# Kernel tuning notes

Hardware: AMD Instinct MI355X
Metric: run time of the kernel (lower is better)

Reference implementation:

```python
import jax, jax.numpy as jnp
import numpy as np

NV = 100000   # vehicle nodes
NE = 100000   # 'edge' nodes (dst type)
E = 250000    # graph edges (connects relation)
VDIM = 16
EDIM = 16
HID = 128
HEADS = 4
DH = 128      # out_feats per head (GATv2Conv(hid, hid))
EPS = 1e-5
NEG_SLOPE = 0.2


def _layernorm(x, g, b):
    mu = x.mean(-1, keepdims=True)
    var = ((x - mu) ** 2).mean(-1, keepdims=True)
    return (x - mu) * jax.lax.rsqrt(var + EPS) * g + b


def setup_inputs() -> dict:
    key = jax.random.key(0)
    ks = jax.random.split(key, 20)
    s = 0.05
    return {
        "v_feat": jax.random.normal(ks[0], (NV, VDIM), jnp.float32),
        "e_feat": jax.random.normal(ks[1], (NE, EDIM), jnp.float32),
        "Wv": jax.random.normal(ks[2], (VDIM, HID), jnp.float32) * s,
        "bv": jnp.zeros((HID,), jnp.float32),
        "gv": jnp.ones((HID,), jnp.float32),
        "betav": jnp.zeros((HID,), jnp.float32),
        "We": jax.random.normal(ks[3], (EDIM, HID), jnp.float32) * s,
        "be": jnp.zeros((HID,), jnp.float32),
        "ge": jnp.ones((HID,), jnp.float32),
        "betae": jnp.zeros((HID,), jnp.float32),
        "Wsrc": jax.random.normal(ks[4], (HID, HEADS * DH), jnp.float32) * s,
        "bsrc": jnp.zeros((HEADS * DH,), jnp.float32),
        "Wdst": jax.random.normal(ks[5], (HID, HEADS * DH), jnp.float32) * s,
        "bdst": jnp.zeros((HEADS * DH,), jnp.float32),
        "attn": jax.random.normal(ks[6], (HEADS, DH), jnp.float32) * s,
        "Wp": jax.random.normal(ks[7], (HID, HID), jnp.float32) * s,
        "bp": jnp.zeros((HID,), jnp.float32),
        "src": jax.random.randint(ks[8], (E,), 0, NV, jnp.int32),
        "dst": jax.random.randint(ks[9], (E,), 0, NE, jnp.int32),
    }


def reference(v_feat, e_feat, Wv, bv, gv, betav, We, be, ge, betae,
              Wsrc, bsrc, Wdst, bdst, attn, Wp, bp, src, dst):
    # --- node-type encoders: Linear -> ReLU -> LayerNorm ---
    h_v = _layernorm(jax.nn.relu(v_feat @ Wv + bv), gv, betav)      # [NV, HID]
    h_e = _layernorm(jax.nn.relu(e_feat @ We + be), ge, betae)      # [NE, HID]

    # --- GATv2Conv (bipartite: vehicle -> edge), 4 heads ---
    fs = (h_v @ Wsrc + bsrc).reshape(NV, HEADS, DH)                 # src proj
    fd = (h_e @ Wdst + bdst).reshape(NE, HEADS, DH)                 # dst proj
    e = jax.nn.leaky_relu(fs[src] + fd[dst], NEG_SLOPE)             # [E, H, D]
    score = jnp.einsum("ehd,hd->eh", e, attn)                       # [E, H]
    # segment-wise (per-dst-node) softmax over incoming edges
    smax = jax.ops.segment_max(score, dst, num_segments=NE)         # [NE, H]
    ex = jnp.exp(score - smax[dst])
    denom = jax.ops.segment_sum(ex, dst, num_segments=NE)
    alpha = ex / denom[dst]                                         # [E, H]
    out = jax.ops.segment_sum(alpha[:, :, None] * fs[src], dst,
                              num_segments=NE)                      # [NE, H, D]

    # HeteroGraphConv mean-aggregate (single relation -> identity),
    # then mean over heads (edge_out.dim()==3 branch)
    edge_out = out.mean(axis=1)                                     # [NE, HID]

    # feature_proj: Linear -> ReLU -> Dropout(eval: identity)
    return jax.nn.relu(edge_out @ Wp + bp)
```

## Files before the change

kernel.cpp:

```cpp
#include <hip/hip_runtime.h>
#include <hip/hip_bf16.h>
#include <math.h>

#define NV 100000
#define NE_N 100000
#define NEDGE 250000
#define NEG 0.2f
#define LN_EPS 1e-5f

typedef __bf16 bf16_t;
typedef __bf16 bf16x8 __attribute__((ext_vector_type(8)));
typedef float f32x4 __attribute__((ext_vector_type(4)));

__device__ inline unsigned short f2bfu(float f) {
    return __builtin_bit_cast(unsigned short, (__bf16)f);
}
__device__ inline float bfu2f(unsigned short u) {
    return (float)__builtin_bit_cast(__bf16, u);
}
__device__ inline float blo(unsigned w) { return __uint_as_float(w << 16); }
__device__ inline float bhi(unsigned w) { return __uint_as_float(w & 0xffff0000u); }
__device__ inline float lrelu(float x) { return x > 0.f ? x : NEG * x; }
__device__ inline unsigned pk2(float a, float b) {
    return (unsigned)f2bfu(a) | ((unsigned)f2bfu(b) << 16);
}

__device__ __forceinline__ void gload_lds16(const bf16_t* g, unsigned short* l) {
    __builtin_amdgcn_global_load_lds(
        (const __attribute__((address_space(1))) unsigned int*)g,
        (__attribute__((address_space(3))) unsigned int*)l,
        16, 0, 0);
}

__global__ __launch_bounds__(256) void prep_kernel(
    const float* __restrict__ Wsrc, const float* __restrict__ Wdst,
    const float* __restrict__ Wp, bf16_t* __restrict__ pS,
    bf16_t* __restrict__ pD, bf16_t* __restrict__ pP)
{
    int t = blockIdx.x * 256 + threadIdx.x;
    if (t < 8192) {
        int ksq = t >> 9, col = t & 511;
#pragma unroll
        for (int j = 0; j < 8; ++j)
            pS[(size_t)t * 8 + j] = (bf16_t)Wsrc[(ksq * 8 + j) * 512 + col];
    } else if (t < 16384) {
        int g = t - 8192;
        int ksq = g >> 9, col = g & 511;
#pragma unroll
        for (int j = 0; j < 8; ++j)
            pD[(size_t)g * 8 + j] = (bf16_t)Wdst[(ksq * 8 + j) * 512 + col];
    } else if (t < 18432) {
        int g = t - 16384;
        int ksq = g >> 7, col = g & 127;
#pragma unroll
        for (int j = 0; j < 8; ++j)
            pP[(size_t)g * 8 + j] = (bf16_t)Wp[(ksq * 8 + j) * 128 + col];
    }
}

__global__ __launch_bounds__(256) void count_kernel(
    const int* __restrict__ dst, int* __restrict__ deg)
{
    int t = blockIdx.x * 256 + threadIdx.x;
    if (t < NEDGE) atomicAdd(&deg[dst[t]], 1);
}

__global__ __launch_bounds__(256) void scan1_kernel(
    const int* __restrict__ deg, int* __restrict__ offs, int* __restrict__ bsum)
{
    __shared__ int s[256];
    int i = blockIdx.x * 256 + threadIdx.x;
    int v = (i < NE_N) ? deg[i] : 0;
    s[threadIdx.x] = v;
    __syncthreads();
    for (int off = 1; off < 256; off <<= 1) {
        int t_ = (threadIdx.x >= off) ? s[threadIdx.x - off] : 0;
        __syncthreads();
        s[threadIdx.x] += t_;
        __syncthreads();
    }
    if (i < NE_N) offs[i] = s[threadIdx.x] - v;
    if (threadIdx.x == 255) bsum[blockIdx.x] = s[255];
}

__global__ __launch_bounds__(512) void scan2_kernel(int* __restrict__ bsum, int nb)
{
    __shared__ int s[512];
    int t = threadIdx.x;
    int v = (t < nb) ? bsum[t] : 0;
    s[t] = v;
    __syncthreads();
    for (int off = 1; off < 512; off <<= 1) {
        int t_ = (t >= off) ? s[t - off] : 0;
        __syncthreads();
        s[t] += t_;
        __syncthreads();
    }
    if (t < nb) bsum[t] = s[t] - v;
}

__global__ __launch_bounds__(256) void scan3_kernel(
    int* __restrict__ offs, const int* __restrict__ bsum, int* __restrict__ cursor)
{
    int i = blockIdx.x * 256 + threadIdx.x;
    if (i < NE_N) {
        int o = offs[i] + bsum[blockIdx.x];
        offs[i] = o;
        cursor[i] = o;
    }
}

__global__ __launch_bounds__(256) void scatter_kernel(
    const int* __restrict__ dst, int* __restrict__ cursor, int* __restrict__ eidx)
{
    int t = blockIdx.x * 256 + threadIdx.x;
    if (t < NEDGE) {
        int pos = atomicAdd(&cursor[dst[t]], 1);
        eidx[pos] = t;
    }
}

__global__ __launch_bounds__(256, 4) void enc_proj_kernel(
    const float* __restrict__ featV, const float* __restrict__ WencV,
    const float* __restrict__ bencV, const float* __restrict__ gV,
    const float* __restrict__ betaV, const bf16_t* __restrict__ ApackV,
    const float* __restrict__ bprojV, unsigned short* __restrict__ outV,
    const float* __restrict__ featE, const float* __restrict__ WencE,
    const float* __restrict__ bencE, const float* __restrict__ gE,
    const float* __restrict__ betaE, const bf16_t* __restrict__ ApackE,
    const float* __restrict__ bprojE, unsigned short* __restrict__ outE,
    int nblk1, int M)
{
    __shared__ unsigned short Hs[64 * 136];
    __shared__ __align__(16) unsigned short Abuf[2][8192];
    __shared__ __align__(16) float Bias[512];

    int b = blockIdx.x;
    bool isV = b < nblk1;
    const float* feat  = isV ? featV  : featE;
    const float* Wenc  = isV ? WencV  : WencE;
    const float* benc  = isV ? bencV  : bencE;
    const float* gln   = isV ? gV     : gE;
    const float* beta  = isV ? betaV  : betaE;
    const bf16_t* Apack = isV ? ApackV : ApackE;
    const float* bproj = isV ? bprojV : bprojE;
    unsigned short* out = isV ? outV : outE;
    int row0 = (isV ? b : b - nblk1) * 64;

    int t = threadIdx.x;
    int l = t & 63;
    int w = t >> 6;
    int rbase = __builtin_amdgcn_readfirstlane(w * 16);

#pragma unroll
    for (int j = 0; j < 4; ++j) {
        int ksq = w * 4 + j;
        gload_lds16(Apack + ((size_t)(ksq * 512) + l) * 8, &Abuf[0][ksq * 512]);
    }
    if (t < 128)
        *(float4*)&Bias[t * 4] = *(const float4*)(bproj + t * 4);

    float wc0[16], wc1[16];
#pragma unroll
    for (int k = 0; k < 16; ++k) {
        float2 wv = *(const float2*)(Wenc + k * 128 + 2 * l);
        wc0[k] = wv.x;
        wc1[k] = wv.y;
    }
    float2 bv2 = *(const float2*)(benc + 2 * l);

#pragma unroll
    for (int i = 0; i < 16; ++i) {
        int grow = row0 + rbase + i;
        if (grow >= M) grow = M - 1;
        const float* fr = feat + (size_t)grow * 16;
        float a0 = bv2.x, a1 = bv2.y;
#pragma unroll
        for (int k = 0; k < 16; ++k) {
            float f = fr[k];
            a0 = fmaf(f, wc0[k], a0);
            a1 = fmaf(f, wc1[k], a1);
        }
        a0 = fmaxf(a0, 0.f);
        a1 = fmaxf(a1, 0.f);
        *(unsigned*)&Hs[(rbase + i) * 136 + 2 * l] = pk2(a0, a1);
    }

    float s = 0.f, s2 = 0.f;
    {
        int rr = rbase + (l >> 2);
        int q = l & 3;
#pragma unroll
        for (int j = 0; j < 4; ++j) {
            uint4 v = *(const uint4*)&Hs[rr * 136 + q * 32 + j * 8];
            float x;
            x = blo(v.x); s += x; s2 = fmaf(x, x, s2);
            x = bhi(v.x); s += x; s2 = fmaf(x, x, s2);
            x = blo(v.y); s += x; s2 = fmaf(x, x, s2);
            x = bhi(v.y); s += x; s2 = fmaf(x, x, s2);
            x = blo(v.z); s += x; s2 = fmaf(x, x, s2);
            x = bhi(v.z); s += x; s2 = fmaf(x, x, s2);
            x = blo(v.w); s += x; s2 = fmaf(x, x, s2);
            x = bhi(v.w); s += x; s2 = fmaf(x, x, s2);
        }
    }
    s  += __shfl_xor(s, 1, 64);  s  += __shfl_xor(s, 2, 64);
    s2 += __shfl_xor(s2, 1, 64); s2 += __shfl_xor(s2, 2, 64);
    float mu  = s * (1.f / 128.f);
    float var = s2 * (1.f / 128.f) - mu * mu;
    float inv = rsqrtf(var + LN_EPS);

    int kq = l >> 4;
    int ln = l & 15;
    float mu_r  = __shfl(mu,  ln * 4, 64);
    float inv_r = __shfl(inv, ln * 4, 64);

    bf16x8 bfr[4];
#pragma unroll
    for (int ks = 0; ks < 4; ++ks) {
        int c0 = ks * 32 + kq * 8;
        uint4 v = *(const uint4*)&Hs[(rbase + ln) * 136 + c0];
        float4 g0 = *(const float4*)(gln + c0);
        float4 g1 = *(const float4*)(gln + c0 + 4);
        float4 b0 = *(const float4*)(beta + c0);
        float4 b1 = *(const float4*)(beta + c0 + 4);
        uint4 p;
        p.x = pk2(fmaf((blo(v.x) - mu_r) * inv_r, g0.x, b0.x),
                  fmaf((bhi(v.x) - mu_r) * inv_r, g0.y, b0.y));
        p.y = pk2(fmaf((blo(v.y) - mu_r) * inv_r, g0.z, b0.z),
                  fmaf((bhi(v.y) - mu_r) * inv_r, g0.w, b0.w));
        p.z = pk2(fmaf((blo(v.z) - mu_r) * inv_r, g1.x, b1.x),
                  fmaf((bhi(v.z) - mu_r) * inv_r, g1.y, b1.y));
        p.w = pk2(fmaf((blo(v.w) - mu_r) * inv_r, g1.z, b1.z),
                  fmaf((bhi(v.w) - mu_r) * inv_r, g1.w, b1.w));
        bfr[ks] = __builtin_bit_cast(bf16x8, p);
    }

    unsigned short* stag = Hs + rbase * 136;
    int node = row0 + rbase + ln;
    bool wr = node < M;

#pragma unroll
    for (int p = 0; p < 8; ++p) {
        if (p == 0)
            asm volatile("s_waitcnt vmcnt(0) lgkmcnt(0)" ::: "memory");
        else
            asm volatile("s_waitcnt vmcnt(2)" ::: "memory");
        __builtin_amdgcn_s_barrier();

        if (p < 7) {
#pragma unroll
            for (int j = 0; j < 4; ++j) {
                int ksq = w * 4 + j;
                gload_lds16(Apack + ((size_t)(ksq * 512 + (p + 1) * 64) + l) * 8,
                            &Abuf[(p + 1) & 1][ksq * 512]);
            }
            __builtin_amdgcn_sched_barrier(0);
        }

        const unsigned short* Ac = Abuf[p & 1];
#pragma unroll
        for (int mt = 0; mt < 4; ++mt) {
            bf16x8 a[4];
#pragma unroll
            for (int ks = 0; ks < 4; ++ks)
                a[ks] = *(const bf16x8*)&Ac[((ks * 4 + kq) * 64 + mt * 16 + ln) * 8];

            f32x4 acc = {0.f, 0.f, 0.f, 0.f};
#pragma unroll
            for (int ks = 0; ks < 4; ++ks)
                acc = __builtin_amdgcn_mfma_f32_16x16x32_bf16(a[ks], bfr[ks], acc, 0, 0, 0);

            int colp = p * 64 + mt * 16 + kq * 4;
            float4 bb = *(const float4*)&Bias[colp];
            ushort4 o;
            o.x = f2bfu(acc[0] + bb.x);
            o.y = f2bfu(acc[1] + bb.y);
            o.z = f2bfu(acc[2] + bb.z);
            o.w = f2bfu(acc[3] + bb.w);
            *(ushort4*)&stag[ln * 136 + mt * 16 + kq * 4] = o;
        }
#pragma unroll
        for (int i = 0; i < 2; ++i) {
            uint4 v = *(const uint4*)&stag[ln * 136 + i * 32 + kq * 8];
            if (wr)
                *(uint4*)(out + (size_t)node * 512 + p * 64 + i * 32 + kq * 8) = v;
        }
    }
}

__global__ __launch_bounds__(256) void final_gemm_kernel(
    const float* __restrict__ A, const bf16_t* __restrict__ Ppack,
    const float* __restrict__ bp, float* __restrict__ C, int M)
{
    __shared__ unsigned short Hs[64 * 136];
    int t = threadIdx.x;
    int lane = t & 63;
    int w = t >> 6;
    int row0 = blockIdx.x * 64;

#pragma unroll
    for (int i = 0; i < 8; ++i) {
        int f4 = i * 256 + t;
        int r = f4 >> 5;
        int c4 = (f4 & 31) * 4;
        float4 v = make_float4(0.f, 0.f, 0.f, 0.f);
        if (row0 + r < M)
            v = ((const float4*)(A + (size_t)(row0 + r) * 128))[f4 & 31];
        ushort4 o;
        o.x = f2bfu(v.x); o.y = f2bfu(v.y); o.z = f2bfu(v.z); o.w = f2bfu(v.w);
        *(ushort4*)&Hs[r * 136 + c4] = o;
    }
    __syncthreads();

    int kq = lane >> 4;
    int ln = lane & 15;

    f32x4 acc[2][4];
#pragma unroll
    for (int mt = 0; mt < 2; ++mt)
#pragma unroll
        for (int nt = 0; nt < 4; ++nt) {
            f32x4 z = {0.f, 0.f, 0.f, 0.f};
            acc[mt][nt] = z;
        }

#pragma unroll
    for (int ks = 0; ks < 4; ++ks) {
        bf16x8 bfr[4];
#pragma unroll
        for (int nt = 0; nt < 4; ++nt) {
            const uint4* p = (const uint4*)&Hs[(nt * 16 + ln) * 136 + ks * 32 + kq * 8];
            bfr[nt] = __builtin_bit_cast(bf16x8, *p);
        }
        bf16x8 afr[2];
#pragma unroll
        for (int mt = 0; mt < 2; ++mt) {
            int colA = w * 32 + mt * 16 + ln;
            afr[mt] = *(const bf16x8*)(Ppack + ((size_t)(ks * 4 + kq) * 128 + colA) * 8);
        }
#pragma unroll
        for (int mt = 0; mt < 2; ++mt)
#pragma unroll
            for (int nt = 0; nt < 4; ++nt)
                acc[mt][nt] = __builtin_amdgcn_mfma_f32_16x16x32_bf16(
                    afr[mt], bfr[nt], acc[mt][nt], 0, 0, 0);
    }

#pragma unroll
    for (int mt = 0; mt < 2; ++mt) {
        int col = w * 32 + mt * 16 + kq * 4;
        float4 bb = *(const float4*)(bp + col);
#pragma unroll
        for (int nt = 0; nt < 4; ++nt) {
            int node = row0 + nt * 16 + ln;
            if (node < M) {
                float4 o;
                o.x = fmaxf(acc[mt][nt][0] + bb.x, 0.f);
                o.y = fmaxf(acc[mt][nt][1] + bb.y, 0.f);
                o.z = fmaxf(acc[mt][nt][2] + bb.z, 0.f);
                o.w = fmaxf(acc[mt][nt][3] + bb.w, 0.f);
                *(float4*)(C + (size_t)node * 128 + col) = o;
            }
        }
    }
}

__global__ __launch_bounds__(256) void softagg_kernel(
    const unsigned short* __restrict__ fs, const unsigned short* __restrict__ fdp,
    const float* __restrict__ attn, const int* __restrict__ src,
    const int* __restrict__ offs, const int* __restrict__ deg,
    const int* __restrict__ eidx, float* __restrict__ out)
{
    int d = blockIdx.x * 4 + (threadIdx.x >> 6);
    if (d >= NE_N) return;
    int l = threadIdx.x & 63;
    int r0 = offs[d];
    int n = deg[d];
    int o = l * 8;

    uint4 fv = *(const uint4*)(fdp + (size_t)d * 512 + o);
    float fdv[8] = { blo(fv.x), bhi(fv.x), blo(fv.y), bhi(fv.y),
                     blo(fv.z), bhi(fv.z), blo(fv.w), bhi(fv.w) };
    float4 w0 = *(const float4*)(attn + o);
    float4 w1 = *(const float4*)(attn + o + 4);
    float wv[8] = { w0.x, w0.y, w0.z, w0.w, w1.x, w1.y, w1.z, w1.w };

    float m = -1e30f, sm = 0.f;
    float acc[8];
#pragma unroll
    for (int j = 0; j < 8; ++j) acc[j] = 0.f;

    for (int base = 0; base < n; base += 64) {
        int cnt = min(n - base, 64);
        int sl = 0;
        if (l < cnt) sl = src[eidx[r0 + base + l]];
        for (int i0 = 0; i0 < cnt; i0 += 4) {
            uint4 av[4];
#pragma unroll
            for (int j = 0; j < 4; ++j) {
                int idx = (i0 + j < cnt) ? i0 + j : cnt - 1;
                int s = __shfl(sl, idx, 64);
                av[j] = *(const uint4*)(fs + (size_t)s * 512 + o);
            }
            int mcnt = min(4, cnt - i0);
#pragma unroll
            for (int j = 0; j < 4; ++j) {
                if (j < mcnt) {
                    float fsv[8] = { blo(av[j].x), bhi(av[j].x),
                                     blo(av[j].y), bhi(av[j].y),
                                     blo(av[j].z), bhi(av[j].z),
                                     blo(av[j].w), bhi(av[j].w) };
                    float p = 0.f;
#pragma unroll
                    for (int jj = 0; jj < 8; ++jj)
                        p = fmaf(lrelu(fsv[jj] + fdv[jj]), wv[jj], p);
#pragma unroll
                    for (int mk = 1; mk < 16; mk <<= 1)
                        p += __shfl_xor(p, mk, 64);
                    float mn = fmaxf(m, p);
                    float c  = __expf(m - mn);
                    float aw = __expf(p - mn);
                    sm = sm * c + aw;
                    m = mn;
#pragma unroll
                    for (int jj = 0; jj < 8; ++jj)
                        acc[jj] = fmaf(aw, fsv[jj], acc[jj] * c);
                }
            }
        }
    }

    float inv = (n > 0) ? 0.25f / sm : 0.f;
#pragma unroll
    for (int j = 0; j < 8; ++j) {
        float v = acc[j] * inv;
        v += __shfl_xor(v, 16, 64);
        v += __shfl_xor(v, 32, 64);
        acc[j] = v;
    }
    if (l < 16) {
        float4 o0 = make_float4(acc[0], acc[1], acc[2], acc[3]);
        float4 o1 = make_float4(acc[4], acc[5], acc[6], acc[7]);
        *(float4*)(out + (size_t)d * 128 + l * 8) = o0;
        *(float4*)(out + (size_t)d * 128 + l * 8 + 4) = o1;
    }
}

extern "C" void kernel_launch(void* const* d_in, const int* in_sizes, int n_in,
                              void* d_out, int out_size, void* d_ws, size_t ws_size,
                              hipStream_t stream)
{
    const float* v_feat = (const float*)d_in[0];
    const float* e_feat = (const float*)d_in[1];
    const float* Wv     = (const float*)d_in[2];
    const float* bv     = (const float*)d_in[3];
    const float* gv     = (const float*)d_in[4];
    const float* betav  = (const float*)d_in[5];
    const float* We     = (const float*)d_in[6];
    const float* be     = (const float*)d_in[7];
    const float* ge     = (const float*)d_in[8];
    const float* betae  = (const float*)d_in[9];
    const float* Wsrc   = (const float*)d_in[10];
    const float* bsrc   = (const float*)d_in[11];
    const float* Wdst   = (const float*)d_in[12];
    const float* bdst   = (const float*)d_in[13];
    const float* attn   = (const float*)d_in[14];
    const float* Wp     = (const float*)d_in[15];
    const float* bp     = (const float*)d_in[16];
    const int*   src    = (const int*)d_in[17];
    const int*   dst    = (const int*)d_in[18];
    float* out = (float*)d_out;

    unsigned short* fs = (unsigned short*)d_ws;
    unsigned short* fd = fs + (size_t)NV * 512;
    int* deg    = (int*)(fd + (size_t)NE_N * 512);
    int* offs   = deg + NE_N;
    int* cursor = offs + NE_N;
    int* bsum   = cursor + NE_N;
    int* eidx   = bsum + 512;
    bf16_t* pS  = (bf16_t*)(eidx + NEDGE);
    bf16_t* pD  = pS + 65536;
    bf16_t* pP  = pD + 65536;

    const int NB_SCAN = (NE_N + 255) / 256;

    prep_kernel<<<72, 256, 0, stream>>>(Wsrc, Wdst, Wp, pS, pD, pP);

    hipMemsetAsync(deg, 0, (size_t)NE_N * sizeof(int), stream);
    count_kernel<<<(NEDGE + 255) / 256, 256, 0, stream>>>(dst, deg);
    scan1_kernel<<<NB_SCAN, 256, 0, stream>>>(deg, offs, bsum);
    scan2_kernel<<<1, 512, 0, stream>>>(bsum, NB_SCAN);
    scan3_kernel<<<NB_SCAN, 256, 0, stream>>>(offs, bsum, cursor);
    scatter_kernel<<<(NEDGE + 255) / 256, 256, 0, stream>>>(dst, cursor, eidx);

    enc_proj_kernel<<<3126, 256, 0, stream>>>(
        v_feat, Wv, bv, gv, betav, pS, bsrc, fs,
        e_feat, We, be, ge, betae, pD, bdst, fd,
        1563, 100000);

    softagg_kernel<<<NE_N / 4, 256, 0, stream>>>(fs, fd, attn, src, offs, deg,
                                                 eidx, out);

    final_gemm_kernel<<<1563, 256, 0, stream>>>(out, pP, bp, out, NE_N);
}
```

Before: 336.6 us.

## Stage encoder input rows via LDS async loads and simplify edge gather loop

The encoder+projection kernel now loads its 64x16 float input tile into shared memory with global_load_lds and reads it back as float4, replacing per-thread scalar global loads. The fs/fd workspace buffers are padded to a multiple of 64 rows, so the bounds check on the output store is dropped. The first wait no longer drains vmcnt. The attention aggregation loop loses its 4-way batched gather of source rows and becomes a simple one-edge-per-iteration loop. That reduces register pressure and branching but gives up memory-level parallelism on the gathers.

```diff
diff --git a/kernel.cpp b/kernel.cpp
--- a/kernel.cpp
+++ b/kernel.cpp
@@ -5,6 +5,7 @@
 #define NV 100000
 #define NE_N 100000
 #define NEDGE 250000
+#define NPAD 100032
 #define NEG 0.2f
 #define LN_EPS 1e-5f
 
@@ -25,7 +26,7 @@
     return (unsigned)f2bfu(a) | ((unsigned)f2bfu(b) << 16);
 }
 
-__device__ __forceinline__ void gload_lds16(const bf16_t* g, unsigned short* l) {
+__device__ __forceinline__ void gload_lds16(const void* g, void* l) {
     __builtin_amdgcn_global_load_lds(
         (const __attribute__((address_space(1))) unsigned int*)g,
         (__attribute__((address_space(3))) unsigned int*)l,
@@ -152,6 +153,12 @@
     int w = t >> 6;
     int rbase = __builtin_amdgcn_readfirstlane(w * 16);
 
+    {
+        int sr = row0 + rbase + (l >> 2);
+        if (sr > M - 1) sr = M - 1;
+        gload_lds16(feat + (size_t)sr * 16 + (l & 3) * 4, &Abuf[1][w * 512]);
+    }
+
 #pragma unroll
     for (int j = 0; j < 4; ++j) {
         int ksq = w * 4 + j;
@@ -169,18 +176,33 @@
     }
     float2 bv2 = *(const float2*)(benc + 2 * l);
 
+    asm volatile("s_waitcnt vmcnt(0)" ::: "memory");
+
+    const float* Fs = (const float*)&Abuf[1][0];
 #pragma unroll
     for (int i = 0; i < 16; ++i) {
-        int grow = row0 + rbase + i;
-        if (grow >= M) grow = M - 1;
-        const float* fr = feat + (size_t)grow * 16;
+        const float* fr = Fs + (rbase + i) * 16;
+        float4 f0 = *(const float4*)(fr);
+        float4 f1 = *(const float4*)(fr + 4);
+        float4 f2 = *(const float4*)(fr + 8);
+        float4 f3 = *(const float4*)(fr + 12);
         float a0 = bv2.x, a1 = bv2.y;
-#pragma unroll
-        for (int k = 0; k < 16; ++k) {
-            float f = fr[k];
-            a0 = fmaf(f, wc0[k], a0);
-            a1 = fmaf(f, wc1[k], a1);
-        }
+        a0 = fmaf(f0.x, wc0[0], a0);  a1 = fmaf(f0.x, wc1[0], a1);
+        a0 = fmaf(f0.y, wc0[1], a0);  a1 = fmaf(f0.y, wc1[1], a1);
+        a0 = fmaf(f0.z, wc0[2], a0);  a1 = fmaf(f0.z, wc1[2], a1);
+        a0 = fmaf(f0.w, wc0[3], a0);  a1 = fmaf(f0.w, wc1[3], a1);
+        a0 = fmaf(f1.x, wc0[4], a0);  a1 = fmaf(f1.x, wc1[4], a1);
+        a0 = fmaf(f1.y, wc0[5], a0);  a1 = fmaf(f1.y, wc1[5], a1);
+        a0 = fmaf(f1.z, wc0[6], a0);  a1 = fmaf(f1.z, wc1[6], a1);
+        a0 = fmaf(f1.w, wc0[7], a0);  a1 = fmaf(f1.w, wc1[7], a1);
+        a0 = fmaf(f2.x, wc0[8], a0);  a1 = fmaf(f2.x, wc1[8], a1);
+        a0 = fmaf(f2.y, wc0[9], a0);  a1 = fmaf(f2.y, wc1[9], a1);
+        a0 = fmaf(f2.z, wc0[10], a0); a1 = fmaf(f2.z, wc1[10], a1);
+        a0 = fmaf(f2.w, wc0[11], a0); a1 = fmaf(f2.w, wc1[11], a1);
+        a0 = fmaf(f3.x, wc0[12], a0); a1 = fmaf(f3.x, wc1[12], a1);
+        a0 = fmaf(f3.y, wc0[13], a0); a1 = fmaf(f3.y, wc1[13], a1);
+        a0 = fmaf(f3.z, wc0[14], a0); a1 = fmaf(f3.z, wc1[14], a1);
+        a0 = fmaf(f3.w, wc0[15], a0); a1 = fmaf(f3.w, wc1[15], a1);
         a0 = fmaxf(a0, 0.f);
         a1 = fmaxf(a1, 0.f);
         *(unsigned*)&Hs[(rbase + i) * 136 + 2 * l] = pk2(a0, a1);
@@ -238,12 +260,11 @@
 
     unsigned short* stag = Hs + rbase * 136;
     int node = row0 + rbase + ln;
-    bool wr = node < M;
 
 #pragma unroll
     for (int p = 0; p < 8; ++p) {
         if (p == 0)
-            asm volatile("s_waitcnt vmcnt(0) lgkmcnt(0)" ::: "memory");
+            asm volatile("s_waitcnt lgkmcnt(0)" ::: "memory");
         else
             asm volatile("s_waitcnt vmcnt(2)" ::: "memory");
         __builtin_amdgcn_s_barrier();
@@ -283,8 +304,7 @@
 #pragma unroll
         for (int i = 0; i < 2; ++i) {
             uint4 v = *(const uint4*)&stag[ln * 136 + i * 32 + kq * 8];
-            if (wr)
-                *(uint4*)(out + (size_t)node * 512 + p * 64 + i * 32 + kq * 8) = v;
+            *(uint4*)(out + (size_t)node * 512 + p * 64 + i * 32 + kq * 8) = v;
         }
     }
 }
@@ -395,39 +415,26 @@
         int cnt = min(n - base, 64);
         int sl = 0;
         if (l < cnt) sl = src[eidx[r0 + base + l]];
-        for (int i0 = 0; i0 < cnt; i0 += 4) {
-            uint4 av[4];
-#pragma unroll
-            for (int j = 0; j < 4; ++j) {
-                int idx = (i0 + j < cnt) ? i0 + j : cnt - 1;
-                int s = __shfl(sl, idx, 64);
-                av[j] = *(const uint4*)(fs + (size_t)s * 512 + o);
-            }
-            int mcnt = min(4, cnt - i0);
-#pragma unroll
-            for (int j = 0; j < 4; ++j) {
-                if (j < mcnt) {
-                    float fsv[8] = { blo(av[j].x), bhi(av[j].x),
-                                     blo(av[j].y), bhi(av[j].y),
-                                     blo(av[j].z), bhi(av[j].z),
-                                     blo(av[j].w), bhi(av[j].w) };
-                    float p = 0.f;
-#pragma unroll
-                    for (int jj = 0; jj < 8; ++jj)
-                        p = fmaf(lrelu(fsv[jj] + fdv[jj]), wv[jj], p);
-#pragma unroll
-                    for (int mk = 1; mk < 16; mk <<= 1)
-                        p += __shfl_xor(p, mk, 64);
-                    float mn = fmaxf(m, p);
-                    float c  = __expf(m - mn);
-                    float aw = __expf(p - mn);
-                    sm = sm * c + aw;
-                    m = mn;
-#pragma unroll
-                    for (int jj = 0; jj < 8; ++jj)
-                        acc[jj] = fmaf(aw, fsv[jj], acc[jj] * c);
-                }
-            }
+        for (int i = 0; i < cnt; ++i) {
+            int s = __shfl(sl, i, 64);
+            uint4 a = *(const uint4*)(fs + (size_t)s * 512 + o);
+            float fsv[8] = { blo(a.x), bhi(a.x), blo(a.y), bhi(a.y),
+                             blo(a.z), bhi(a.z), blo(a.w), bhi(a.w) };
+            float p = 0.f;
+#pragma unroll
+            for (int j = 0; j < 8; ++j)
+                p = fmaf(lrelu(fsv[j] + fdv[j]), wv[j], p);
+#pragma unroll
+            for (int mk = 1; mk < 16; mk <<= 1)
+                p += __shfl_xor(p, mk, 64);
+            float mn = fmaxf(m, p);
+            float c  = __expf(m - mn);
+            float av = __expf(p - mn);
+            sm = sm * c + av;
+            m = mn;
+#pragma unroll
+            for (int j = 0; j < 8; ++j)
+                acc[j] = fmaf(av, fsv[j], acc[j] * c);
         }
     }
 
@@ -473,8 +480,8 @@
     float* out = (float*)d_out;
 
     unsigned short* fs = (unsigned short*)d_ws;
-    unsigned short* fd = fs + (size_t)NV * 512;
-    int* deg    = (int*)(fd + (size_t)NE_N * 512);
+    unsigned short* fd = fs + (size_t)NPAD * 512;
+    int* deg    = (int*)(fd + (size_t)NPAD * 512);
     int* offs   = deg + NE_N;
     int* cursor = offs + NE_N;
     int* bsum   = cursor + NE_N;
```

Result: faster. 297.7 us (-11.6%).
